# Performance work log

Hardware: AMD Instinct MI355X
Metric: run time of the kernel (lower is better)

## Reference

```python
import jax, jax.numpy as jnp
import numpy as np

KD, KY, KX = 3, 3, 3  # kernel_size from init_kwargs


def setup_inputs() -> dict:
    key = jax.random.key(0)
    x = jax.random.normal(key, (4, 2, 64, 256, 256), dtype=jnp.float32)
    return {"x": x}


def reference(x):
    # x: [B, CH, D, H, W]
    B, CH, D, H, W = x.shape
    pd, py, px = (KD - 1) // 2, (KY - 1) // 2, (KX - 1) // 2
    # replicate padding (torch F.pad mode='replicate' == jnp.pad mode='edge')
    xp = jnp.pad(x, ((0, 0), (0, 0), (pd, pd), (py, py), (px, px)), mode='edge')
    center = (KD * KY * KX) // 2  # flattened center position, excluded from max
    # running max over the 26 non-center neighbors; never materializes the
    # [B, CH, 27, D, H, W] tensor the torch conv3d path creates.
    max_nc = jnp.full(x.shape, -jnp.inf, dtype=x.dtype)
    idx = 0
    for i in range(KD):
        for j in range(KY):
            for k in range(KX):
                if idx != center:
                    shifted = xp[:, :, i:i + D, j:j + H, k:k + W]
                    max_nc = jnp.maximum(max_nc, shifted)
                idx += 1
    mask = x > max_nc  # strict local maximum (excluding self)
    return x * mask.astype(x.dtype)
```

## Files before the change

### kernel.cpp

```cpp
#include <hip/hip_runtime.h>


constexpr int D_   = 64;
constexpr int H_   = 256;
constexpr int W_   = 256;
constexpr int HW_  = H_ * W_;
constexpr int NVOL = 8;
constexpr int DC   = 16;

__device__ __forceinline__ float f3(float a, float b, float c) {
    return fmaxf(fmaxf(a, b), c);
}

__global__ __launch_bounds__(256, 4)
void nms3d(const float* __restrict__ x, float* __restrict__ out)
{
    const int tx = threadIdx.x;
    const int ty = threadIdx.y;
    const int h  = (blockIdx.y << 2) + ty;
    const int n  = blockIdx.z;
    const int z0 = blockIdx.x * DC;

    const float* __restrict__ base  = x   + (size_t)n * D_ * HW_;
    float* __restrict__       obase = out + (size_t)n * D_ * HW_;

    const int r0 = (h == 0)      ? 0      : h - 1;
    const int r2 = (h == H_ - 1) ? H_ - 1 : h + 1;
    const int c  = tx << 2;

    float4 vm9_pp = make_float4(0.f, 0.f, 0.f, 0.f);
    float4 vm9_p  = make_float4(0.f, 0.f, 0.f, 0.f);
    float4 cr8_p  = make_float4(0.f, 0.f, 0.f, 0.f);
    float4 vprev  = make_float4(0.f, 0.f, 0.f, 0.f);

    for (int zi = z0 - 1; zi <= z0 + DC; ++zi) {
        const int zc = min(max(zi, 0), D_ - 1);
        const float* sp = base + (size_t)zc * HW_;

        const float4 a = *(const float4*)(sp + r0 * W_ + c);
        const float4 b = *(const float4*)(sp + h  * W_ + c);
        const float4 d = *(const float4*)(sp + r2 * W_ + c);

        float aL = __shfl_up(a.w, 1);   if (tx == 0)  aL = a.x;
        float bL = __shfl_up(b.w, 1);   if (tx == 0)  bL = b.x;
        float dL = __shfl_up(d.w, 1);   if (tx == 0)  dL = d.x;
        float aR = __shfl_down(a.x, 1); if (tx == 63) aR = a.w;
        float bR = __shfl_down(b.x, 1); if (tx == 63) bR = b.w;
        float dR = __shfl_down(d.x, 1); if (tx == 63) dR = d.w;

        float4 ha, hb, hd, nb;
        ha.x = f3(aL, a.x, a.y);  ha.y = f3(a.x, a.y, a.z);
        ha.z = f3(a.y, a.z, a.w); ha.w = f3(a.z, a.w, aR);
        hb.x = f3(bL, b.x, b.y);  hb.y = f3(b.x, b.y, b.z);
        hb.z = f3(b.y, b.z, b.w); hb.w = f3(b.z, b.w, bR);
        hd.x = f3(dL, d.x, d.y);  hd.y = f3(d.x, d.y, d.z);
        hd.z = f3(d.y, d.z, d.w); hd.w = f3(d.z, d.w, dR);
        nb.x = fmaxf(bL, b.y);  nb.y = fmaxf(b.x, b.z);
        nb.z = fmaxf(b.y, b.w); nb.w = fmaxf(b.z, bR);

        float4 cur, c8;
        cur.x = f3(ha.x, hb.x, hd.x); cur.y = f3(ha.y, hb.y, hd.y);
        cur.z = f3(ha.z, hb.z, hd.z); cur.w = f3(ha.w, hb.w, hd.w);
        c8.x  = f3(ha.x, hd.x, nb.x); c8.y  = f3(ha.y, hd.y, nb.y);
        c8.z  = f3(ha.z, hd.z, nb.z); c8.w  = f3(ha.w, hd.w, nb.w);

        if (zi > z0) {
            float4 mx, o;
            mx.x = f3(vm9_pp.x, cr8_p.x, cur.x);
            mx.y = f3(vm9_pp.y, cr8_p.y, cur.y);
            mx.z = f3(vm9_pp.z, cr8_p.z, cur.z);
            mx.w = f3(vm9_pp.w, cr8_p.w, cur.w);
            o.x = vprev.x > mx.x ? vprev.x : 0.0f;
            o.y = vprev.y > mx.y ? vprev.y : 0.0f;
            o.z = vprev.z > mx.z ? vprev.z : 0.0f;
            o.w = vprev.w > mx.w ? vprev.w : 0.0f;
            *(float4*)(obase + (size_t)(zi - 1) * HW_ + (size_t)h * W_ + c) = o;
        }
        vm9_pp = vm9_p; vm9_p = cur; cr8_p = c8; vprev = b;
    }
}

extern "C" void kernel_launch(void* const* d_in, const int* in_sizes, int n_in,
                              void* d_out, int out_size, void* d_ws, size_t ws_size,
                              hipStream_t stream)
{
    const float* x = (const float*)d_in[0];
    float* out = (float*)d_out;
    dim3 block(64, 4, 1);
    dim3 grid(D_ / DC, H_ / 4, NVOL);
    nms3d<<<grid, block, 0, stream>>>(x, out);
}
```

Baseline: 239.0 us.

## Prefetch next depth slice, fully unroll loop, share vertical max to cut shuffles

The depth chunk shrinks from 16 to 8 slices and the z loop is fully unrolled. The next slice's three rows are loaded one iteration ahead, so global-load latency overlaps the current slice's max computation. The max of the rows above and below is now taken before the horizontal pass, which cuts shuffles from six to four and removes several fmax ops. The cost is a higher halo-reload ratio from the smaller chunk and more register pressure from the prefetch and unrolling.

```diff
diff --git a/kernel.cpp b/kernel.cpp
--- a/kernel.cpp
+++ b/kernel.cpp
@@ -6,7 +6,7 @@
 constexpr int W_   = 256;
 constexpr int HW_  = H_ * W_;
 constexpr int NVOL = 8;
-constexpr int DC   = 16;
+constexpr int DC   = 8;
 
 __device__ __forceinline__ float f3(float a, float b, float c) {
     return fmaxf(fmaxf(a, b), c);
@@ -28,41 +28,51 @@
     const int r2 = (h == H_ - 1) ? H_ - 1 : h + 1;
     const int c  = tx << 2;
 
+    {
+        const int zc = max(z0 - 1, 0);
+        const float* sp = base + (size_t)zc * HW_;
+    }
+    const float* sp0 = base + (size_t)max(z0 - 1, 0) * HW_;
+    float4 a = *(const float4*)(sp0 + r0 * W_ + c);
+    float4 b = *(const float4*)(sp0 + h  * W_ + c);
+    float4 d = *(const float4*)(sp0 + r2 * W_ + c);
+
     float4 vm9_pp = make_float4(0.f, 0.f, 0.f, 0.f);
     float4 vm9_p  = make_float4(0.f, 0.f, 0.f, 0.f);
     float4 cr8_p  = make_float4(0.f, 0.f, 0.f, 0.f);
     float4 vprev  = make_float4(0.f, 0.f, 0.f, 0.f);
 
-    for (int zi = z0 - 1; zi <= z0 + DC; ++zi) {
-        const int zc = min(max(zi, 0), D_ - 1);
-        const float* sp = base + (size_t)zc * HW_;
+#pragma unroll
+    for (int t = 0; t < DC + 2; ++t) {
+        const int zi = z0 - 1 + t;
 
-        const float4 a = *(const float4*)(sp + r0 * W_ + c);
-        const float4 b = *(const float4*)(sp + h  * W_ + c);
-        const float4 d = *(const float4*)(sp + r2 * W_ + c);
+        const int zn = min(zi + 1, D_ - 1);
+        const float* spn = base + (size_t)zn * HW_;
+        const float4 an = *(const float4*)(spn + r0 * W_ + c);
+        const float4 bn = *(const float4*)(spn + h  * W_ + c);
+        const float4 dn = *(const float4*)(spn + r2 * W_ + c);
 
-        float aL = __shfl_up(a.w, 1);   if (tx == 0)  aL = a.x;
-        float bL = __shfl_up(b.w, 1);   if (tx == 0)  bL = b.x;
-        float dL = __shfl_up(d.w, 1);   if (tx == 0)  dL = d.x;
-        float aR = __shfl_down(a.x, 1); if (tx == 63) aR = a.w;
-        float bR = __shfl_down(b.x, 1); if (tx == 63) bR = b.w;
-        float dR = __shfl_down(d.x, 1); if (tx == 63) dR = d.w;
+        float4 va;
+        va.x = fmaxf(a.x, d.x); va.y = fmaxf(a.y, d.y);
+        va.z = fmaxf(a.z, d.z); va.w = fmaxf(a.w, d.w);
 
-        float4 ha, hb, hd, nb;
-        ha.x = f3(aL, a.x, a.y);  ha.y = f3(a.x, a.y, a.z);
-        ha.z = f3(a.y, a.z, a.w); ha.w = f3(a.z, a.w, aR);
-        hb.x = f3(bL, b.x, b.y);  hb.y = f3(b.x, b.y, b.z);
-        hb.z = f3(b.y, b.z, b.w); hb.w = f3(b.z, b.w, bR);
-        hd.x = f3(dL, d.x, d.y);  hd.y = f3(d.x, d.y, d.z);
-        hd.z = f3(d.y, d.z, d.w); hd.w = f3(d.z, d.w, dR);
+        float vaL = __shfl_up(va.w, 1);  if (tx == 0)  vaL = va.x;
+        float vaR = __shfl_down(va.x, 1);if (tx == 63) vaR = va.w;
+        float bL  = __shfl_up(b.w, 1);   if (tx == 0)  bL  = b.x;
+        float bR  = __shfl_down(b.x, 1); if (tx == 63) bR  = b.w;
+
+        float4 hv;
+        hv.x = f3(vaL, va.x, va.y);  hv.y = f3(va.x, va.y, va.z);
+        hv.z = f3(va.y, va.z, va.w); hv.w = f3(va.z, va.w, vaR);
+        float4 nb;
         nb.x = fmaxf(bL, b.y);  nb.y = fmaxf(b.x, b.z);
         nb.z = fmaxf(b.y, b.w); nb.w = fmaxf(b.z, bR);
 
-        float4 cur, c8;
-        cur.x = f3(ha.x, hb.x, hd.x); cur.y = f3(ha.y, hb.y, hd.y);
-        cur.z = f3(ha.z, hb.z, hd.z); cur.w = f3(ha.w, hb.w, hd.w);
-        c8.x  = f3(ha.x, hd.x, nb.x); c8.y  = f3(ha.y, hd.y, nb.y);
-        c8.z  = f3(ha.z, hd.z, nb.z); c8.w  = f3(ha.w, hd.w, nb.w);
+        float4 c8, cur;
+        c8.x  = fmaxf(hv.x, nb.x); c8.y  = fmaxf(hv.y, nb.y);
+        c8.z  = fmaxf(hv.z, nb.z); c8.w  = fmaxf(hv.w, nb.w);
+        cur.x = fmaxf(c8.x, b.x);  cur.y = fmaxf(c8.y, b.y);
+        cur.z = fmaxf(c8.z, b.z);  cur.w = fmaxf(c8.w, b.w);
 
         if (zi > z0) {
             float4 mx, o;
@@ -77,6 +87,7 @@
             *(float4*)(obase + (size_t)(zi - 1) * HW_ + (size_t)h * W_ + c) = o;
         }
         vm9_pp = vm9_p; vm9_p = cur; cr8_p = c8; vprev = b;
+        a = an; b = bn; d = dn;
     }
 }
 
```

Result: faster. 231.1 us (-3.3%).

## Stream along H instead of D with unrolled register sliding window

Applied to the files above, without the earlier changes.

Each thread now owns one depth slice and walks down 16 rows of H, keeping a sliding window of three depth planes' row maxima in registers. Before, it owned one row and streamed through 16 depth slices. The next row is prefetched one step ahead inside a fully unrolled loop, which is meant to add memory-level parallelism and cut halo re-reads along depth. In exchange each row is loaded from three planes, so there is redundant traffic across the four z-threads of a block, and the unrolling adds register pressure.

```diff
diff --git a/kernel.cpp b/kernel.cpp
--- a/kernel.cpp
+++ b/kernel.cpp
@@ -6,10 +6,21 @@
 constexpr int W_   = 256;
 constexpr int HW_  = H_ * W_;
 constexpr int NVOL = 8;
-constexpr int DC   = 16;
+constexpr int HSEG = 16;
 
 __device__ __forceinline__ float f3(float a, float b, float c) {
     return fmaxf(fmaxf(a, b), c);
+}
+
+__device__ __forceinline__ void rowfold(const float4 r, int tx,
+                                        float4& hm, float4& nb)
+{
+    float rL = __shfl_up(r.w, 1);   if (tx == 0)  rL = r.x;
+    float rR = __shfl_down(r.x, 1); if (tx == 63) rR = r.w;
+    hm.x = f3(rL, r.x, r.y);  hm.y = f3(r.x, r.y, r.z);
+    hm.z = f3(r.y, r.z, r.w); hm.w = f3(r.z, r.w, rR);
+    nb.x = fmaxf(rL, r.y);    nb.y = fmaxf(r.x, r.z);
+    nb.z = fmaxf(r.y, r.w);   nb.w = fmaxf(r.z, rR);
 }
 
 __global__ __launch_bounds__(256, 4)
@@ -17,66 +28,60 @@
 {
     const int tx = threadIdx.x;
     const int ty = threadIdx.y;
-    const int h  = (blockIdx.y << 2) + ty;
+    const int z  = (blockIdx.x << 2) + ty;
+    const int h0 = blockIdx.y * HSEG;
     const int n  = blockIdx.z;
-    const int z0 = blockIdx.x * DC;
-
-    const float* __restrict__ base  = x   + (size_t)n * D_ * HW_;
-    float* __restrict__       obase = out + (size_t)n * D_ * HW_;
-
-    const int r0 = (h == 0)      ? 0      : h - 1;
-    const int r2 = (h == H_ - 1) ? H_ - 1 : h + 1;
     const int c  = tx << 2;
 
-    float4 vm9_pp = make_float4(0.f, 0.f, 0.f, 0.f);
-    float4 vm9_p  = make_float4(0.f, 0.f, 0.f, 0.f);
-    float4 cr8_p  = make_float4(0.f, 0.f, 0.f, 0.f);
-    float4 vprev  = make_float4(0.f, 0.f, 0.f, 0.f);
+    const float* __restrict__ base = x + (size_t)n * D_ * HW_;
+    const float* __restrict__ pm = base + (size_t)max(z - 1, 0)      * HW_;
+    const float* __restrict__ pc = base + (size_t)z                  * HW_;
+    const float* __restrict__ pp = base + (size_t)min(z + 1, D_ - 1) * HW_;
+    float* __restrict__ ob = out + (size_t)n * D_ * HW_ + (size_t)z * HW_;
 
-    for (int zi = z0 - 1; zi <= z0 + DC; ++zi) {
-        const int zc = min(max(zi, 0), D_ - 1);
-        const float* sp = base + (size_t)zc * HW_;
+    const int r0 = max(h0 - 1, 0) * W_ + c;
+    float4 rm = *(const float4*)(pm + r0);
+    float4 rc = *(const float4*)(pc + r0);
+    float4 rp = *(const float4*)(pp + r0);
 
-        const float4 a = *(const float4*)(sp + r0 * W_ + c);
-        const float4 b = *(const float4*)(sp + h  * W_ + c);
-        const float4 d = *(const float4*)(sp + r2 * W_ + c);
+    float4 m0 = {0,0,0,0}, m1 = {0,0,0,0};
+    float4 c0 = {0,0,0,0}, c1 = {0,0,0,0};
+    float4 p0 = {0,0,0,0}, p1 = {0,0,0,0};
+    float4 nb1 = {0,0,0,0}, b1 = {0,0,0,0};
 
-        float aL = __shfl_up(a.w, 1);   if (tx == 0)  aL = a.x;
-        float bL = __shfl_up(b.w, 1);   if (tx == 0)  bL = b.x;
-        float dL = __shfl_up(d.w, 1);   if (tx == 0)  dL = d.x;
-        float aR = __shfl_down(a.x, 1); if (tx == 63) aR = a.w;
-        float bR = __shfl_down(b.x, 1); if (tx == 63) bR = b.w;
-        float dR = __shfl_down(d.x, 1); if (tx == 63) dR = d.w;
+#pragma unroll
+    for (int t = 0; t < HSEG + 2; ++t) {
+        float4 rmn, rcn, rpn;
+        if (t <= HSEG) {
+            const int rn = min(h0 + t, H_ - 1) * W_ + c;
+            rmn = *(const float4*)(pm + rn);
+            rcn = *(const float4*)(pc + rn);
+            rpn = *(const float4*)(pp + rn);
+        }
 
-        float4 ha, hb, hd, nb;
-        ha.x = f3(aL, a.x, a.y);  ha.y = f3(a.x, a.y, a.z);
-        ha.z = f3(a.y, a.z, a.w); ha.w = f3(a.z, a.w, aR);
-        hb.x = f3(bL, b.x, b.y);  hb.y = f3(b.x, b.y, b.z);
-        hb.z = f3(b.y, b.z, b.w); hb.w = f3(b.z, b.w, bR);
-        hd.x = f3(dL, d.x, d.y);  hd.y = f3(d.x, d.y, d.z);
-        hd.z = f3(d.y, d.z, d.w); hd.w = f3(d.z, d.w, dR);
-        nb.x = fmaxf(bL, b.y);  nb.y = fmaxf(b.x, b.z);
-        nb.z = fmaxf(b.y, b.w); nb.w = fmaxf(b.z, bR);
+        float4 m2, p2, c2, nb2, dum;
+        rowfold(rm, tx, m2, dum);
+        rowfold(rp, tx, p2, dum);
+        rowfold(rc, tx, c2, nb2);
 
-        float4 cur, c8;
-        cur.x = f3(ha.x, hb.x, hd.x); cur.y = f3(ha.y, hb.y, hd.y);
-        cur.z = f3(ha.z, hb.z, hd.z); cur.w = f3(ha.w, hb.w, hd.w);
-        c8.x  = f3(ha.x, hd.x, nb.x); c8.y  = f3(ha.y, hd.y, nb.y);
-        c8.z  = f3(ha.z, hd.z, nb.z); c8.w  = f3(ha.w, hd.w, nb.w);
+        if (t >= 2) {
+            float4 mx, o;
+            mx.x = f3(f3(m0.x, m1.x, m2.x), f3(p0.x, p1.x, p2.x), f3(c0.x, c2.x, nb1.x));
+            mx.y = f3(f3(m0.y, m1.y, m2.y), f3(p0.y, p1.y, p2.y), f3(c0.y, c2.y, nb1.y));
+            mx.z = f3(f3(m0.z, m1.z, m2.z), f3(p0.z, p1.z, p2.z), f3(c0.z, c2.z, nb1.z));
+            mx.w = f3(f3(m0.w, m1.w, m2.w), f3(p0.w, p1.w, p2.w), f3(c0.w, c2.w, nb1.w));
+            o.x = b1.x > mx.x ? b1.x : 0.0f;
+            o.y = b1.y > mx.y ? b1.y : 0.0f;
+            o.z = b1.z > mx.z ? b1.z : 0.0f;
+            o.w = b1.w > mx.w ? b1.w : 0.0f;
+            *(float4*)(ob + (size_t)(h0 + t - 2) * W_ + c) = o;
+        }
 
-        if (zi > z0) {
-            float4 mx, o;
-            mx.x = f3(vm9_pp.x, cr8_p.x, cur.x);
-            mx.y = f3(vm9_pp.y, cr8_p.y, cur.y);
-            mx.z = f3(vm9_pp.z, cr8_p.z, cur.z);
-            mx.w = f3(vm9_pp.w, cr8_p.w, cur.w);
-            o.x = vprev.x > mx.x ? vprev.x : 0.0f;
-            o.y = vprev.y > mx.y ? vprev.y : 0.0f;
-            o.z = vprev.z > mx.z ? vprev.z : 0.0f;
-            o.w = vprev.w > mx.w ? vprev.w : 0.0f;
-            *(float4*)(obase + (size_t)(zi - 1) * HW_ + (size_t)h * W_ + c) = o;
-        }
-        vm9_pp = vm9_p; vm9_p = cur; cr8_p = c8; vprev = b;
+        m0 = m1; m1 = m2;
+        c0 = c1; c1 = c2;
+        p0 = p1; p1 = p2;
+        nb1 = nb2; b1 = rc;
+        rm = rmn; rc = rcn; rp = rpn;
     }
 }
 
@@ -87,6 +92,6 @@
     const float* x = (const float*)d_in[0];
     float* out = (float*)d_out;
     dim3 block(64, 4, 1);
-    dim3 grid(D_ / DC, H_ / 4, NVOL);
+    dim3 grid(D_ / 4, H_ / HSEG, NVOL);
     nms3d<<<grid, block, 0, stream>>>(x, out);
 }
```

Result: slower. 245.4 us (+2.7%).
